# Performance work log

Measured on AMD Instinct MI355X. Metric: run time of the kernel, lower is better.

## Reference

```python
import jax, jax.numpy as jnp
import numpy as np

DIM = 2048
N_HEADS = 16
Q_LORA = 1536
KV_LORA = 512
NOPE = 128
ROPE = 64
QK_D = NOPE + ROPE  # 192
V_D = 128
EPS = 1e-6
B, S = 2, 2048


def rmsnorm(x, w, eps=EPS):
    return x * jax.lax.rsqrt(jnp.mean(x * x, axis=-1, keepdims=True) + eps) * w


def rotate_pe(x, cos, sin):
    # x: [B, S, H, ROPE]; cos/sin: [S, ROPE] -> broadcast [1, S, 1, ROPE]
    c = cos[None, :, None, :]
    s = sin[None, :, None, :]
    x1, x2 = jnp.split(x, 2, axis=-1)
    rot = jnp.concatenate([-x2, x1], axis=-1)
    return x * c + rot * s


def setup_inputs() -> dict:
    key = jax.random.key(0)
    ks = jax.random.split(key, 8)
    std = 0.02
    x = jax.random.normal(ks[0], (B, S, DIM), dtype=jnp.float32)
    # proper rotary tables
    inv_freq = 1.0 / (10000.0 ** (np.arange(0, ROPE, 2, dtype=np.float32) / ROPE))
    t = np.arange(S, dtype=np.float32)
    freqs = np.outer(t, inv_freq)  # [S, ROPE/2]
    emb = np.concatenate([freqs, freqs], axis=-1)  # [S, ROPE]
    cos = jnp.asarray(np.cos(emb))
    sin = jnp.asarray(np.sin(emb))
    wq_a = jax.random.normal(ks[1], (Q_LORA, DIM), dtype=jnp.float32) * std
    q_norm_w = jnp.ones((Q_LORA,), dtype=jnp.float32)
    wq_b = jax.random.normal(ks[2], (N_HEADS * QK_D, Q_LORA), dtype=jnp.float32) * std
    wkv_a = jax.random.normal(ks[3], (KV_LORA + ROPE, DIM), dtype=jnp.float32) * std
    kv_norm_w = jnp.ones((KV_LORA,), dtype=jnp.float32)
    wkv_b = jax.random.normal(ks[4], (N_HEADS * (NOPE + V_D), KV_LORA), dtype=jnp.float32) * std
    wo = jax.random.normal(ks[5], (DIM, N_HEADS * V_D), dtype=jnp.float32) * std
    return {"x": x, "cos": cos, "sin": sin, "wq_a": wq_a, "q_norm_w": q_norm_w,
            "wq_b": wq_b, "wkv_a": wkv_a, "kv_norm_w": kv_norm_w, "wkv_b": wkv_b, "wo": wo}


def mla_forward(x, cos, sin, wq_a, q_norm_w, wq_b, wkv_a, kv_norm_w, wkv_b, wo):
    bsz, seqlen, _ = x.shape
    scale = QK_D ** (-0.5)
    # Q path: low-rank down-proj -> RMSNorm -> up-proj
    q = rmsnorm(x @ wq_a.T, q_norm_w) @ wq_b.T
    q = q.reshape(bsz, seqlen, N_HEADS, QK_D)
    q_nope, q_pe = q[..., :NOPE], q[..., NOPE:]
    q_pe = rotate_pe(q_pe, cos, sin)
    q = jnp.concatenate([q_nope, q_pe], axis=-1)
    # KV path: shared low-rank latent + single rope slice
    kv = x @ wkv_a.T  # [B, S, KV_LORA + ROPE]
    kv_c, k_pe = kv[..., :KV_LORA], kv[..., KV_LORA:]
    k_pe = rotate_pe(k_pe[:, :, None, :], cos, sin)  # [B, S, 1, ROPE]
    kvb = rmsnorm(kv_c, kv_norm_w) @ wkv_b.T
    kvb = kvb.reshape(bsz, seqlen, N_HEADS, NOPE + V_D)
    k_nope, v = kvb[..., :NOPE], kvb[..., NOPE:]
    k = jnp.concatenate([k_nope, jnp.broadcast_to(k_pe, (bsz, seqlen, N_HEADS, ROPE))], axis=-1)
    # causal attention
    scores = jnp.einsum('bqhd,bkhd->bhqk', q, k) * scale
    mask = jnp.tril(jnp.ones((seqlen, seqlen), dtype=bool))
    scores = jnp.where(mask[None, None], scores, jnp.finfo(scores.dtype).min)
    p = jax.nn.softmax(scores, axis=-1)
    out = jnp.einsum('bhqk,bkhd->bqhd', p, v)
    out = out.reshape(bsz, seqlen, N_HEADS * V_D)
    return out @ wo.T


def reference(x, cos, sin, wq_a, q_norm_w, wq_b, wkv_a, kv_norm_w, wkv_b, wo):
    return mla_forward(x, cos, sin, wq_a, q_norm_w, wq_b, wkv_a, kv_norm_w, wkv_b, wo)
```

## Files before the change

### kernel.cpp

```cpp
#include <hip/hip_runtime.h>

typedef unsigned short u16;
typedef __attribute__((ext_vector_type(8))) short short8;
typedef __attribute__((ext_vector_type(4))) float floatx4;

__device__ __forceinline__ float bf2f(u16 u) {
  union { unsigned int i; float f; } v; v.i = ((unsigned int)u) << 16; return v.f;
}
__device__ __forceinline__ u16 f2bf(float f) {
  union { float f; unsigned int i; } v; v.f = f;
  unsigned int u = v.i;
  u += 0x7fffu + ((u >> 16) & 1u);
  return (u16)(u >> 16);
}

__device__ __forceinline__ void gld_lds16(const void* g, void* l) {
  __builtin_amdgcn_global_load_lds(
      (const __attribute__((address_space(1))) unsigned int*)g,
      (__attribute__((address_space(3))) unsigned int*)l, 16, 0, 0);
}

#define SBAR()   __builtin_amdgcn_s_barrier()
#define SCHED0() __builtin_amdgcn_sched_barrier(0)

__global__ __launch_bounds__(256) void repack_all_k(
    const float* __restrict__ x, const float* __restrict__ wqa,
    const float* __restrict__ wkva, const float* __restrict__ wqb,
    const float* __restrict__ wkvb, const float* __restrict__ wo,
    u16* __restrict__ xb, u16* __restrict__ wcat, u16* __restrict__ wqbb,
    u16* __restrict__ wkbb, u16* __restrict__ wob) {
  long i = ((long)blockIdx.x * 256 + threadIdx.x) * 4;
  int region = blockIdx.y;
  const float* s = nullptr; u16* d = nullptr; long n = 0;
  switch (region) {
    case 0: s = x;    d = xb;   n = 4096L * 2048; break;
    case 1: s = nullptr; d = wcat; n = 2176L * 2048; break;
    case 2: s = wqb;  d = wqbb; n = 3072L * 1536; break;
    case 3: s = wkvb; d = wkbb; n = 4096L * 512;  break;
    case 4: s = wo;   d = wob;  n = 2048L * 2048; break;
  }
  if (i >= n) return;
  float4 v;
  if (region == 1) {
    long r = i >> 11, c = i & 2047;
    if (r < 1536)      v = *(const float4*)(wqa + r * 2048 + c);
    else if (r < 2112) v = *(const float4*)(wkva + (r - 1536) * 2048 + c);
    else               v = (float4){0.f, 0.f, 0.f, 0.f};
  } else {
    v = *(const float4*)(s + i);
  }
  d[i + 0] = f2bf(v.x); d[i + 1] = f2bf(v.y);
  d[i + 2] = f2bf(v.z); d[i + 3] = f2bf(v.w);
}

template <int OUT_F32>
__device__ __forceinline__ void gemm_tile(
    const u16* __restrict__ A, int lda, const u16* __restrict__ W, int ldw,
    void* __restrict__ Cv, int ldc, int K, int bm, int bn,
    u16* Asm, u16* Bsm) {
  int tid = threadIdx.x;
  int lane = tid & 63, w = tid >> 6;
  int wm = (w >> 1) * 64, wn = (w & 1) * 64;

  floatx4 acc[4][4];
#pragma unroll
  for (int i = 0; i < 4; i++)
#pragma unroll
    for (int j = 0; j < 4; j++) acc[i][j] = (floatx4){0.f, 0.f, 0.f, 0.f};

  int sr = lane >> 2;
  int sc = (lane & 3) * 8;
  int fr = lane & 15;
  int fq = (lane >> 4) * 8;

  for (int k0 = 0; k0 < K; k0 += 32) {
#pragma unroll
    for (int c = 0; c < 2; c++) {
      int row = 32 * w + 16 * c + sr;
      gld_lds16(A + (size_t)(bm + row) * lda + k0 + sc, &Asm[(32 * w + 16 * c) * 32]);
      gld_lds16(W + (size_t)(bn + row) * ldw + k0 + sc, &Bsm[(32 * w + 16 * c) * 32]);
    }
    __syncthreads();
    short8 af[4], bfr[4];
#pragma unroll
    for (int i = 0; i < 4; i++)
      af[i] = *(const short8*)&Asm[(wm + i * 16 + fr) * 32 + fq];
#pragma unroll
    for (int j = 0; j < 4; j++)
      bfr[j] = *(const short8*)&Bsm[(wn + j * 16 + fr) * 32 + fq];
#pragma unroll
    for (int i = 0; i < 4; i++)
#pragma unroll
      for (int j = 0; j < 4; j++)
        acc[i][j] = __builtin_amdgcn_mfma_f32_16x16x32_bf16(af[i], bfr[j], acc[i][j], 0, 0, 0);
    __syncthreads();
  }

  int cr = (lane >> 4) * 4, cc = lane & 15;
#pragma unroll
  for (int i = 0; i < 4; i++)
#pragma unroll
    for (int j = 0; j < 4; j++) {
      int col = bn + wn + j * 16 + cc;
#pragma unroll
      for (int r = 0; r < 4; r++) {
        size_t row = (size_t)(bm + wm + i * 16 + cr + r);
        if (OUT_F32) ((float*)Cv)[row * ldc + col] = acc[i][j][r];
        else         ((u16*)Cv)[row * ldc + col] = f2bf(acc[i][j][r]);
      }
    }
}

template <int OUT_F32>
__global__ __launch_bounds__(256) void gemm_bt_mfma(
    const u16* __restrict__ A, int lda,
    const u16* __restrict__ W, int ldw,
    void* __restrict__ Cv, int ldc, int K) {
  __shared__ u16 Asm[128 * 32];
  __shared__ u16 Bsm[128 * 32];
  gemm_tile<OUT_F32>(A, lda, W, ldw, Cv, ldc, K, blockIdx.y * 128, blockIdx.x * 128, Asm, Bsm);
}

__global__ __launch_bounds__(256) void gemm_dual_mfma(
    const u16* __restrict__ A1, int lda1, const u16* __restrict__ W1, int ldw1,
    u16* __restrict__ C1, int ldc1, int K1, int nt1,
    const u16* __restrict__ A2, int lda2, const u16* __restrict__ W2, int ldw2,
    u16* __restrict__ C2, int ldc2, int K2) {
  __shared__ u16 Asm[128 * 32];
  __shared__ u16 Bsm[128 * 32];
  int bx = blockIdx.x;
  if (bx < nt1)
    gemm_tile<0>(A1, lda1, W1, ldw1, C1, ldc1, K1, blockIdx.y * 128, bx * 128, Asm, Bsm);
  else
    gemm_tile<0>(A2, lda2, W2, ldw2, C2, ldc2, K2, blockIdx.y * 128, (bx - nt1) * 128, Asm, Bsm);
}

#define GPHASE(LAc, LBc, QQ, STAGE_STMT, WAIT_STMT)                              \
  {                                                                              \
    short8 a00 = *(const short8*)&(LAc)[agbase + (2*(QQ)) * 1024 + g0];          \
    short8 a01 = *(const short8*)&(LAc)[agbase + (2*(QQ)) * 1024 + g1];          \
    short8 a10 = *(const short8*)&(LAc)[agbase + (2*(QQ)+1) * 1024 + g0];        \
    short8 a11 = *(const short8*)&(LAc)[agbase + (2*(QQ)+1) * 1024 + g1];        \
    if ((QQ) == 0) {                                                             \
      _Pragma("unroll")                                                          \
      for (int fj = 0; fj < 4; ++fj) {                                           \
        bfrg[fj][0] = *(const short8*)&(LBc)[bgbase + fj * 1024 + g0];           \
        bfrg[fj][1] = *(const short8*)&(LBc)[bgbase + fj * 1024 + g1];           \
      }                                                                          \
    }                                                                            \
    STAGE_STMT;                                                                  \
    WAIT_STMT;                                                                   \
    SCHED0();                                                                    \
    SBAR();                                                                      \
    asm volatile("s_waitcnt lgkmcnt(0)" ::: "memory");                           \
    SCHED0();                                                                    \
    __builtin_amdgcn_s_setprio(1);                                               \
    _Pragma("unroll")                                                            \
    for (int fj = 0; fj < 4; ++fj) {                                             \
      acc[2*(QQ)][fj]   = __builtin_amdgcn_mfma_f32_16x16x32_bf16(a00, bfrg[fj][0], acc[2*(QQ)][fj],   0, 0, 0); \
      acc[2*(QQ)][fj]   = __builtin_amdgcn_mfma_f32_16x16x32_bf16(a01, bfrg[fj][1], acc[2*(QQ)][fj],   0, 0, 0); \
      acc[2*(QQ)+1][fj] = __builtin_amdgcn_mfma_f32_16x16x32_bf16(a10, bfrg[fj][0], acc[2*(QQ)+1][fj], 0, 0, 0); \
      acc[2*(QQ)+1][fj] = __builtin_amdgcn_mfma_f32_16x16x32_bf16(a11, bfrg[fj][1], acc[2*(QQ)+1][fj], 0, 0, 0); \
    }                                                                            \
    __builtin_amdgcn_s_setprio(0);                                               \
    SCHED0();                                                                    \
    SBAR();                                                                      \
  }

template <int OUT_F32>
__device__ __forceinline__ void gemm256_tile(
    const u16* __restrict__ A, int lda, const u16* __restrict__ W, int ldw,
    void* __restrict__ Cv, int ldc, int K, int bm, int bn,
    u16* __restrict__ LA, u16* __restrict__ LB) {
  int tid = threadIdx.x;
  int lane = tid & 63, w = tid >> 6;
  int wr = w >> 2, wc = w & 3;
  int fr = lane & 15, fq = lane >> 4;

  int srow = lane >> 3;
  int sgl  = (lane & 7) ^ srow;

  int agbase = (wr * 128 + fr) * 64;
  int bgbase = (wc * 64 + fr) * 64;
  int g0 = ((0 * 4 + fq) ^ (fr & 7)) * 8;
  int g1 = ((1 * 4 + fq) ^ (fr & 7)) * 8;

  floatx4 acc[8][4];
#pragma unroll
  for (int i = 0; i < 8; i++)
#pragma unroll
    for (int j = 0; j < 4; j++) acc[i][j] = (floatx4){0.f, 0.f, 0.f, 0.f};

  auto stA = [&](int buf, int kt, int half) {
#pragma unroll
    for (int j = 0; j < 2; ++j) {
      int rbase = half * 128 + (w * 2 + j) * 8;
      gld_lds16(A + (size_t)(bm + rbase + srow) * lda + kt * 64 + sgl * 8,
                (void*)&LA[buf * 16384 + rbase * 64]);
    }
  };
  auto stB = [&](int buf, int kt, int half) {
#pragma unroll
    for (int j = 0; j < 2; ++j) {
      int rbase = half * 128 + (w * 2 + j) * 8;
      gld_lds16(W + (size_t)(bn + rbase + srow) * ldw + kt * 64 + sgl * 8,
                (void*)&LB[buf * 16384 + rbase * 64]);
    }
  };

  const u16* LA0 = LA;           const u16* LB0 = LB;
  const u16* LA1 = LA + 16384;   const u16* LB1 = LB + 16384;

  stB(0, 0, 0); stB(0, 0, 1);
  stA(0, 0, 0); stA(0, 0, 1);
  stB(1, 1, 0); stB(1, 1, 1);
  asm volatile("s_waitcnt vmcnt(4)" ::: "memory");
  SCHED0();
  SBAR();

  int NI = K >> 7;
  for (int i = 0; i < NI; ++i) {
    bool notlast = (i + 1 < NI);
    int t0 = 2 * i;
    {
      short8 bfrg[4][2];
      GPHASE(LA0, LB0, 0, stA(1, t0 + 1, 0), );
      GPHASE(LA0, LB0, 1, stA(1, t0 + 1, 1), );
      GPHASE(LA0, LB0, 2, if (notlast) stB(0, t0 + 2, 0), );
      GPHASE(LA0, LB0, 3, if (notlast) stB(0, t0 + 2, 1),
             if (notlast) { asm volatile("s_waitcnt vmcnt(4)" ::: "memory"); }
             else         { asm volatile("s_waitcnt vmcnt(0)" ::: "memory"); });
    }
    {
      short8 bfrg[4][2];
      GPHASE(LA1, LB1, 0, if (notlast) stA(0, t0 + 2, 0), );
      GPHASE(LA1, LB1, 1, if (notlast) stA(0, t0 + 2, 1), );
      GPHASE(LA1, LB1, 2, if (notlast) stB(1, t0 + 3, 0), );
      GPHASE(LA1, LB1, 3, if (notlast) stB(1, t0 + 3, 1),
             if (notlast) { asm volatile("s_waitcnt vmcnt(4)" ::: "memory"); });
    }
  }

  int cr = (lane >> 4) * 4, cc = lane & 15;
#pragma unroll
  for (int fi = 0; fi < 8; ++fi)
#pragma unroll
    for (int fj = 0; fj < 4; ++fj) {
      int col = bn + wc * 64 + fj * 16 + cc;
#pragma unroll
      for (int r = 0; r < 4; ++r) {
        size_t row = (size_t)(bm + wr * 128 + fi * 16 + cr + r);
        if (OUT_F32) ((float*)Cv)[row * ldc + col] = acc[fi][fj][r];
        else         ((u16*)Cv)[row * ldc + col] = f2bf(acc[fi][fj][r]);
      }
    }
}

template <int OUT_F32>
__global__ __launch_bounds__(512, 2) void gemm256_k(
    const u16* __restrict__ A, int lda,
    const u16* __restrict__ W, int ldw,
    void* __restrict__ Cv, int ldc, int K) {
  __shared__ __align__(16) u16 LAs[2][256 * 64];
  __shared__ __align__(16) u16 LBs[2][256 * 64];
  gemm256_tile<OUT_F32>(A, lda, W, ldw, Cv, ldc, K,
                        blockIdx.y * 256, blockIdx.x * 256, &LAs[0][0], &LBs[0][0]);
}

__global__ __launch_bounds__(256) void normrope_k(
    u16* __restrict__ qkv, const float* __restrict__ qnw,
    const float* __restrict__ kvnw, const float* __restrict__ cosb,
    const float* __restrict__ sinb, int S) {
  int row = blockIdx.x, tid = threadIdx.x;
  u16* p = qkv + (size_t)row * 2176;
  float s1 = 0.f, s2 = 0.f;
#pragma unroll
  for (int it = 0; it < 6; it++) { float v = bf2f(p[tid + 256 * it]); s1 += v * v; }
#pragma unroll
  for (int it = 0; it < 2; it++) { float v = bf2f(p[1536 + tid + 256 * it]); s2 += v * v; }
  for (int off = 32; off > 0; off >>= 1) {
    s1 += __shfl_down(s1, off);
    s2 += __shfl_down(s2, off);
  }
  __shared__ float red1[4], red2[4];
  if ((tid & 63) == 0) { red1[tid >> 6] = s1; red2[tid >> 6] = s2; }
  __syncthreads();
  float inv1 = rsqrtf((red1[0] + red1[1] + red1[2] + red1[3]) / 1536.f + 1e-6f);
  float inv2 = rsqrtf((red2[0] + red2[1] + red2[2] + red2[3]) / 512.f + 1e-6f);
#pragma unroll
  for (int it = 0; it < 6; it++) {
    int i = tid + 256 * it;
    p[i] = f2bf(bf2f(p[i]) * inv1 * qnw[i]);
  }
#pragma unroll
  for (int it = 0; it < 2; it++) {
    int i = tid + 256 * it;
    p[1536 + i] = f2bf(bf2f(p[1536 + i]) * inv2 * kvnw[i]);
  }
  if (tid < 32) {
    int pos = row % S;
    float c1 = cosb[pos * 64 + tid];
    float c2 = cosb[pos * 64 + tid + 32];
    float sn1 = sinb[pos * 64 + tid];
    float sn2 = sinb[pos * 64 + tid + 32];
    float x1 = bf2f(p[2048 + tid]), x2 = bf2f(p[2048 + tid + 32]);
    p[2048 + tid]      = f2bf(x1 * c1 - x2 * sn1);
    p[2048 + tid + 32] = f2bf(x2 * c2 + x1 * sn2);
  }
}

__global__ __launch_bounds__(256) void rope_k(
    u16* __restrict__ base, int row_stride, int head_stride, int head_off,
    const float* __restrict__ cosb, const float* __restrict__ sinb, int S) {
  int t = blockIdx.x;
  int h = blockIdx.y * 8 + (threadIdx.x >> 5);
  int i = threadIdx.x & 31;
  int pos = t % S;
  u16* p = base + (size_t)t * row_stride + h * head_stride + head_off;
  float c1 = cosb[pos * 64 + i];
  float c2 = cosb[pos * 64 + i + 32];
  float s1 = sinb[pos * 64 + i];
  float s2 = sinb[pos * 64 + i + 32];
  float x1 = bf2f(p[i]), x2 = bf2f(p[i + 32]);
  p[i]      = f2bf(x1 * c1 - x2 * s1);
  p[i + 32] = f2bf(x2 * c2 + x1 * s2);
}

__global__ __launch_bounds__(256) void vtrans_k(
    const u16* __restrict__ kvb, u16* __restrict__ vt, int S) {
  int tb = blockIdx.x, h = blockIdx.y, b = blockIdx.z;
  __shared__ __align__(16) u16 Ts[64][136];
  int tid = threadIdx.x;
#pragma unroll
  for (int it = 0; it < 4; it++) {
    int e = tid + 256 * it;
    int tok = e >> 4, c = e & 15;
    short8 v = *(const short8*)(kvb + (size_t)(b * S + tb * 64 + tok) * 4096 + h * 256 + 128 + c * 8);
    *(short8*)&Ts[tok][c * 8] = v;
  }
  __syncthreads();
  int vd = tid >> 1, half = (tid & 1) * 32;
  u16 tmp[32];
#pragma unroll
  for (int j = 0; j < 32; j++) tmp[j] = Ts[half + j][vd];
  u16* dst = vt + ((size_t)((b * 16 + h) * 128) + vd) * S + tb * 64 + half;
#pragma unroll
  for (int c = 0; c < 4; c++)
    *(short8*)(dst + c * 8) = *(short8*)&tmp[c * 8];
}

#define AT_BK 64
__global__ __launch_bounds__(256) void attn_mfma(
    const u16* __restrict__ qf, const u16* __restrict__ kvb,
    const u16* __restrict__ kpe, int kpe_stride, const u16* __restrict__ vt,
    u16* __restrict__ at, int S) {
  int id = blockIdx.x;
  int pair = id >> 5, hb = id & 31;
  int h = hb & 15, b = hb >> 4;
  int NT = S / AT_BK;
  int tid = threadIdx.x, lane = tid & 63, w = tid >> 6;
  int fr = lane & 15, fq = lane >> 4;
  int fs = fr & 7;

  __shared__ __align__(16) u16 Ksn[AT_BK * 128];
  __shared__ __align__(16) u16 Ksp[AT_BK * 64];
  __shared__ __align__(16) u16 Vts[128 * AT_BK];
  __shared__ __align__(16) u16 Ps[64 * AT_BK];

  const float scale = 0.10411804518038971f;

  for (int p = 0; p < 2; p++) {
    int qt = p ? (NT - 1 - pair) : pair;
    int q0 = qt * 64;

    short8 qfrag[6];
    {
      const u16* qrow = qf + (size_t)(b * S + q0 + w * 16 + fr) * 3072 + h * 192 + fq * 8;
#pragma unroll
      for (int ks = 0; ks < 6; ks++) qfrag[ks] = *(const short8*)(qrow + ks * 32);
    }

    floatx4 acc_o[8];
#pragma unroll
    for (int j = 0; j < 8; j++) acc_o[j] = (floatx4){0.f, 0.f, 0.f, 0.f};
    float m_r[4], l_r[4];
#pragma unroll
    for (int r = 0; r < 4; r++) { m_r[r] = -3e38f; l_r[r] = 0.f; }

    for (int kt = 0; kt <= qt; kt++) {
      int k0 = kt * AT_BK;
      size_t tokbase = (size_t)(b * S + k0);
#pragma unroll
      for (int c = 0; c < 4; c++) {
        int row = w * 16 + c * 4 + (lane >> 4);
        int cg = (lane & 15) ^ (row & 7);
        gld_lds16(kvb + (tokbase + row) * 4096 + h * 256 + cg * 8,
                  &Ksn[(w * 16 + c * 4) * 128]);
      }
#pragma unroll
      for (int c = 0; c < 2; c++) {
        int row = w * 16 + c * 8 + (lane >> 3);
        int cg = (lane & 7) ^ (row & 7);
        gld_lds16(kpe + (tokbase + row) * kpe_stride + cg * 8,
                  &Ksp[(w * 16 + c * 8) * 64]);
      }
#pragma unroll
      for (int c = 0; c < 4; c++) {
        int vd = w * 32 + c * 8 + (lane >> 3);
        int cg = (lane & 7) ^ (vd & 7);
        gld_lds16(vt + ((size_t)((b * 16 + h) * 128) + vd) * S + k0 + cg * 8,
                  &Vts[(w * 32 + c * 8) * 64]);
      }
      __syncthreads();

      floatx4 accs[4];
#pragma unroll
      for (int nt = 0; nt < 4; nt++) accs[nt] = (floatx4){0.f, 0.f, 0.f, 0.f};
      __builtin_amdgcn_s_setprio(1);
#pragma unroll
      for (int nt = 0; nt < 4; nt++) {
#pragma unroll
        for (int ks = 0; ks < 4; ks++) {
          short8 bf = *(const short8*)&Ksn[(nt * 16 + fr) * 128 + ((ks * 4 + fq) ^ fs) * 8];
          accs[nt] = __builtin_amdgcn_mfma_f32_16x16x32_bf16(qfrag[ks], bf, accs[nt], 0, 0, 0);
        }
#pragma unroll
        for (int ks = 0; ks < 2; ks++) {
          short8 bf = *(const short8*)&Ksp[(nt * 16 + fr) * 64 + ((ks * 4 + fq) ^ fs) * 8];
          accs[nt] = __builtin_amdgcn_mfma_f32_16x16x32_bf16(qfrag[4 + ks], bf, accs[nt], 0, 0, 0);
        }
      }
      __builtin_amdgcn_s_setprio(0);

      bool diag = (kt == qt);
#pragma unroll
      for (int nt = 0; nt < 4; nt++)
#pragma unroll
        for (int r = 0; r < 4; r++) {
          float s = accs[nt][r] * scale;
          if (diag) {
            int col = nt * 16 + fr;
            int row = fq * 4 + r;
            if (k0 + col > q0 + w * 16 + row) s = -3e38f;
          }
          accs[nt][r] = s;
        }

      float mx4[4];
      int grow = 0;
#pragma unroll
      for (int r = 0; r < 4; r++) {
        float mx = fmaxf(fmaxf(accs[0][r], accs[1][r]), fmaxf(accs[2][r], accs[3][r]));
        mx = fmaxf(mx, __shfl_xor(mx, 1));
        mx = fmaxf(mx, __shfl_xor(mx, 2));
        mx = fmaxf(mx, __shfl_xor(mx, 4));
        mx = fmaxf(mx, __shfl_xor(mx, 8));
        mx4[r] = mx;
        grow |= (mx > m_r[r] + 8.f) ? 1 : 0;
      }
      bool resc = __any(grow);
      float alpha[4];
      if (resc) {
#pragma unroll
        for (int r = 0; r < 4; r++) {
          float mnew = fmaxf(m_r[r], mx4[r]);
          alpha[r] = exp2f(m_r[r] - mnew);
          m_r[r] = mnew;
          l_r[r] *= alpha[r];
        }
      }
#pragma unroll
      for (int nt = 0; nt < 4; nt++)
#pragma unroll
        for (int r = 0; r < 4; r++) {
          float pv = exp2f(accs[nt][r] - m_r[r]);
          l_r[r] += pv;
          int row_p = w * 16 + fq * 4 + r;
          int col = nt * 16 + fr;
          Ps[row_p * 64 + (((col >> 3) ^ (row_p & 7)) * 8) + (col & 7)] = f2bf(pv);
        }
      __syncthreads();

      if (resc) {
#pragma unroll
        for (int j = 0; j < 8; j++)
#pragma unroll
          for (int r = 0; r < 4; r++) acc_o[j][r] *= alpha[r];
      }
      short8 pf0 = *(const short8*)&Ps[(w * 16 + fr) * 64 + (fq ^ fs) * 8];
      short8 pf1 = *(const short8*)&Ps[(w * 16 + fr) * 64 + ((4 + fq) ^ fs) * 8];
      __builtin_amdgcn_s_setprio(1);
#pragma unroll
      for (int j = 0; j < 8; j++) {
        short8 v0 = *(const short8*)&Vts[(j * 16 + fr) * 64 + (fq ^ fs) * 8];
        short8 v1 = *(const short8*)&Vts[(j * 16 + fr) * 64 + ((4 + fq) ^ fs) * 8];
        acc_o[j] = __builtin_amdgcn_mfma_f32_16x16x32_bf16(pf0, v0, acc_o[j], 0, 0, 0);
        acc_o[j] = __builtin_amdgcn_mfma_f32_16x16x32_bf16(pf1, v1, acc_o[j], 0, 0, 0);
      }
      __builtin_amdgcn_s_setprio(0);
      __syncthreads();
    }

    float inv_l[4];
#pragma unroll
    for (int r = 0; r < 4; r++) {
      float sm = l_r[r];
      sm += __shfl_xor(sm, 1);
      sm += __shfl_xor(sm, 2);
      sm += __shfl_xor(sm, 4);
      sm += __shfl_xor(sm, 8);
      inv_l[r] = 1.f / sm;
    }
#pragma unroll
    for (int j = 0; j < 8; j++)
#pragma unroll
      for (int r = 0; r < 4; r++) {
        size_t row = (size_t)(b * S + q0 + w * 16 + fq * 4 + r);
        at[row * 2048 + h * 128 + j * 16 + fr] = f2bf(acc_o[j][r] * inv_l[r]);
      }
  }
}

extern "C" void kernel_launch(void* const* d_in, const int* in_sizes, int n_in,
                              void* d_out, int out_size, void* d_ws, size_t ws_size,
                              hipStream_t stream) {
  (void)in_sizes; (void)n_in; (void)out_size; (void)ws_size;
  const float* x     = (const float*)d_in[0];
  const float* cosb  = (const float*)d_in[1];
  const float* sinb  = (const float*)d_in[2];
  const float* wq_a  = (const float*)d_in[3];
  const float* qnw   = (const float*)d_in[4];
  const float* wq_b  = (const float*)d_in[5];
  const float* wkv_a = (const float*)d_in[6];
  const float* kvnw  = (const float*)d_in[7];
  const float* wkv_b = (const float*)d_in[8];
  const float* wo    = (const float*)d_in[9];
  float* out = (float*)d_out;
  const int B = 2, S = 2048, T = B * S;

  char* wsb = (char*)d_ws;
  size_t off = 0;
  u16* xb   = (u16*)(wsb + off); off += (size_t)T * 2048 * 2;
  u16* wcat = (u16*)(wsb + off); off += (size_t)2176 * 2048 * 2;
  u16* wqbb = (u16*)(wsb + off); off += (size_t)3072 * 1536 * 2;
  u16* wkbb = (u16*)(wsb + off); off += (size_t)4096 * 512 * 2;
  u16* wob  = (u16*)(wsb + off); off += (size_t)2048 * 2048 * 2;
  u16* qkv  = (u16*)(wsb + off); off += (size_t)T * 2176 * 2;
  u16* qf   = (u16*)(wsb + off); off += (size_t)T * 3072 * 2;
  u16* kvb  = (u16*)(wsb + off); off += (size_t)T * 4096 * 2;
  u16* at   = (u16*)(wsb + off); off += (size_t)T * 2048 * 2;
  u16* vt   = xb;

  repack_all_k<<<dim3(8192, 5), 256, 0, stream>>>(
      x, wq_a, wkv_a, wq_b, wkv_b, wo, xb, wcat, wqbb, wkbb, wob);

  gemm_bt_mfma<0><<<dim3(2176 / 128, T / 128), 256, 0, stream>>>(xb, 2048, wcat, 2048, qkv, 2176, 2048);
  normrope_k<<<T, 256, 0, stream>>>(qkv, qnw, kvnw, cosb, sinb, S);
  gemm_dual_mfma<<<dim3(3072 / 128 + 4096 / 128, T / 128), 256, 0, stream>>>(
      qkv, 2176, wqbb, 1536, qf, 3072, 1536, 3072 / 128,
      qkv + 1536, 2176, wkbb, 512, kvb, 4096, 512);
  rope_k<<<dim3(T, 2), 256, 0, stream>>>(qf, 3072, 192, 128, cosb, sinb, S);
  vtrans_k<<<dim3(S / 64, 16, B), 256, 0, stream>>>(kvb, vt, S);
  attn_mfma<<<dim3((S / 128) * 32), 256, 0, stream>>>(qf, kvb, qkv + 2048, 2176, vt, at, S);
  gemm256_k<1><<<dim3(2048 / 256, T / 256), 512, 0, stream>>>(at, 2048, wob, 2048, out, 2048, 2048);
}
```

Before: 480.4 us.

## Double-buffer K/V tiles in attention and reuse rope-K buffer for P

The attention kernel now keeps two LDS buffers for the K-nope, K-rope and V^T tiles. It prefetches the next key tile (or the first tile of the second query tile) with direct global-to-LDS loads while the current tile is being computed. The P matrix is written into the already-consumed K-rope buffer, and the block-wide barrier after the softmax is replaced by a per-wave lgkmcnt wait, since each wave reads back only its own P rows. The softmax switches from exp2f with a log2e-folded scale to __expf with the plain scale, which may add a multiply per exponential. Doubling the LDS footprint could lower occupancy.

```diff
diff --git a/kernel.cpp b/kernel.cpp
--- a/kernel.cpp
+++ b/kernel.cpp
@@ -362,12 +362,43 @@
   int fr = lane & 15, fq = lane >> 4;
   int fs = fr & 7;
 
-  __shared__ __align__(16) u16 Ksn[AT_BK * 128];
-  __shared__ __align__(16) u16 Ksp[AT_BK * 64];
-  __shared__ __align__(16) u16 Vts[128 * AT_BK];
-  __shared__ __align__(16) u16 Ps[64 * AT_BK];
-
-  const float scale = 0.10411804518038971f;
+  __shared__ __align__(16) u16 Ksn[2][AT_BK * 128];
+  __shared__ __align__(16) u16 Ksp[2][AT_BK * 64];
+  __shared__ __align__(16) u16 Vts[2][128 * AT_BK];
+
+  const float scale = 0.07216878364870323f;
+  const size_t vbase = (size_t)((b * 16 + h) * 128);
+
+  auto stage = [&](u16* Kn, u16* Kp, u16* Vt, size_t tokbase, int k0v) {
+#pragma unroll
+    for (int c = 0; c < 4; c++) {
+      int row = w * 16 + c * 4 + (lane >> 4);
+      int cg = (lane & 15) ^ (row & 7);
+      gld_lds16(kvb + (tokbase + row) * 4096 + h * 256 + cg * 8,
+                &Kn[(w * 16 + c * 4) * 128]);
+    }
+#pragma unroll
+    for (int c = 0; c < 2; c++) {
+      int row = w * 16 + c * 8 + (lane >> 3);
+      int cg = (lane & 7) ^ (row & 7);
+      gld_lds16(kpe + (tokbase + row) * kpe_stride + cg * 8,
+                &Kp[(w * 16 + c * 8) * 64]);
+    }
+#pragma unroll
+    for (int c = 0; c < 4; c++) {
+      int vd = w * 32 + c * 8 + (lane >> 3);
+      int cg = (lane & 7) ^ (vd & 7);
+      gld_lds16(vt + (vbase + vd) * S + k0v + cg * 8,
+                &Vt[(w * 32 + c * 8) * 64]);
+    }
+  };
+
+  int cur = 0;
+  stage(Ksn[0], Ksp[0], Vts[0], (size_t)(b * S), 0);
+  asm volatile("s_waitcnt vmcnt(0)" ::: "memory");
+  SCHED0();
+  SBAR();
+  SCHED0();
 
   for (int p = 0; p < 2; p++) {
     int qt = p ? (NT - 1 - pair) : pair;
@@ -389,29 +420,13 @@
 
     for (int kt = 0; kt <= qt; kt++) {
       int k0 = kt * AT_BK;
-      size_t tokbase = (size_t)(b * S + k0);
-#pragma unroll
-      for (int c = 0; c < 4; c++) {
-        int row = w * 16 + c * 4 + (lane >> 4);
-        int cg = (lane & 15) ^ (row & 7);
-        gld_lds16(kvb + (tokbase + row) * 4096 + h * 256 + cg * 8,
-                  &Ksn[(w * 16 + c * 4) * 128]);
-      }
-#pragma unroll
-      for (int c = 0; c < 2; c++) {
-        int row = w * 16 + c * 8 + (lane >> 3);
-        int cg = (lane & 7) ^ (row & 7);
-        gld_lds16(kpe + (tokbase + row) * kpe_stride + cg * 8,
-                  &Ksp[(w * 16 + c * 8) * 64]);
-      }
-#pragma unroll
-      for (int c = 0; c < 4; c++) {
-        int vd = w * 32 + c * 8 + (lane >> 3);
-        int cg = (lane & 7) ^ (vd & 7);
-        gld_lds16(vt + ((size_t)((b * 16 + h) * 128) + vd) * S + k0 + cg * 8,
-                  &Vts[(w * 32 + c * 8) * 64]);
-      }
-      __syncthreads();
+      u16* kn_c = Ksn[cur]; u16* kp_c = Ksp[cur]; u16* vt_c = Vts[cur];
+
+      if (kt < qt)
+        stage(Ksn[cur ^ 1], Ksp[cur ^ 1], Vts[cur ^ 1],
+              (size_t)(b * S + k0 + AT_BK), k0 + AT_BK);
+      else if (p == 0)
+        stage(Ksn[cur ^ 1], Ksp[cur ^ 1], Vts[cur ^ 1], (size_t)(b * S), 0);
 
       floatx4 accs[4];
 #pragma unroll
@@ -421,16 +436,20 @@
       for (int nt = 0; nt < 4; nt++) {
 #pragma unroll
         for (int ks = 0; ks < 4; ks++) {
-          short8 bf = *(const short8*)&Ksn[(nt * 16 + fr) * 128 + ((ks * 4 + fq) ^ fs) * 8];
+          short8 bf = *(const short8*)&kn_c[(nt * 16 + fr) * 128 + ((ks * 4 + fq) ^ fs) * 8];
           accs[nt] = __builtin_amdgcn_mfma_f32_16x16x32_bf16(qfrag[ks], bf, accs[nt], 0, 0, 0);
         }
 #pragma unroll
         for (int ks = 0; ks < 2; ks++) {
-          short8 bf = *(const short8*)&Ksp[(nt * 16 + fr) * 64 + ((ks * 4 + fq) ^ fs) * 8];
+          short8 bf = *(const short8*)&kp_c[(nt * 16 + fr) * 64 + ((ks * 4 + fq) ^ fs) * 8];
           accs[nt] = __builtin_amdgcn_mfma_f32_16x16x32_bf16(qfrag[4 + ks], bf, accs[nt], 0, 0, 0);
         }
       }
       __builtin_amdgcn_s_setprio(0);
+      SCHED0();
+      SBAR();
+      SCHED0();
+      u16* Ps = kp_c;
 
       bool diag = (kt == qt);
 #pragma unroll
@@ -464,7 +483,7 @@
 #pragma unroll
         for (int r = 0; r < 4; r++) {
           float mnew = fmaxf(m_r[r], mx4[r]);
-          alpha[r] = exp2f(m_r[r] - mnew);
+          alpha[r] = __expf(m_r[r] - mnew);
           m_r[r] = mnew;
           l_r[r] *= alpha[r];
         }
@@ -473,13 +492,14 @@
       for (int nt = 0; nt < 4; nt++)
 #pragma unroll
         for (int r = 0; r < 4; r++) {
-          float pv = exp2f(accs[nt][r] - m_r[r]);
+          float pv = __expf(accs[nt][r] - m_r[r]);
           l_r[r] += pv;
           int row_p = w * 16 + fq * 4 + r;
           int col = nt * 16 + fr;
           Ps[row_p * 64 + (((col >> 3) ^ (row_p & 7)) * 8) + (col & 7)] = f2bf(pv);
         }
-      __syncthreads();
+      asm volatile("s_waitcnt lgkmcnt(0)" ::: "memory");
+      SCHED0();
 
       if (resc) {
 #pragma unroll
@@ -492,13 +512,19 @@
       __builtin_amdgcn_s_setprio(1);
 #pragma unroll
       for (int j = 0; j < 8; j++) {
-        short8 v0 = *(const short8*)&Vts[(j * 16 + fr) * 64 + (fq ^ fs) * 8];
-        short8 v1 = *(const short8*)&Vts[(j * 16 + fr) * 64 + ((4 + fq) ^ fs) * 8];
+        short8 v0 = *(const short8*)&vt_c[(j * 16 + fr) * 64 + (fq ^ fs) * 8];
+        short8 v1 = *(const short8*)&vt_c[(j * 16 + fr) * 64 + ((4 + fq) ^ fs) * 8];
         acc_o[j] = __builtin_amdgcn_mfma_f32_16x16x32_bf16(pf0, v0, acc_o[j], 0, 0, 0);
         acc_o[j] = __builtin_amdgcn_mfma_f32_16x16x32_bf16(pf1, v1, acc_o[j], 0, 0, 0);
       }
       __builtin_amdgcn_s_setprio(0);
-      __syncthreads();
+
+      SCHED0();
+      asm volatile("s_waitcnt vmcnt(0)" ::: "memory");
+      SCHED0();
+      SBAR();
+      SCHED0();
+      cur ^= 1;
     }
 
     float inv_l[4];
```

After: 528.4 us. 10.0% more time.

## Prefetch next K/V tiles into LDS during attention compute with split barriers

Applied to the files above, without the earlier changes.

Moves the K-nope/K-pe loads for the next key tile to just after the QK^T MFMAs, and the V loads to just after the PV MFMAs, replacing __syncthreads with explicit waitcnt and s_barrier placement. The aim is to overlap global-to-LDS transfers with softmax and MFMA work instead of stalling at the top of each iteration. It also switches the softmax from a pre-folded log2e scale with exp2f to plain scale with __expf, which adds a multiply per element. The hand-counted vmcnt values and prefetch across passes are fragile if the load counts change.

```diff
diff --git a/kernel.cpp b/kernel.cpp
--- a/kernel.cpp
+++ b/kernel.cpp
@@ -367,7 +367,41 @@
   __shared__ __align__(16) u16 Vts[128 * AT_BK];
   __shared__ __align__(16) u16 Ps[64 * AT_BK];
 
-  const float scale = 0.10411804518038971f;
+  const float scale = 0.07216878364870323f;
+  const size_t vbase = (size_t)((b * 16 + h) * 128);
+
+  auto stageK = [&](size_t tokbase) {
+#pragma unroll
+    for (int c = 0; c < 4; c++) {
+      int row = w * 16 + c * 4 + (lane >> 4);
+      int cg = (lane & 15) ^ (row & 7);
+      gld_lds16(kvb + (tokbase + row) * 4096 + h * 256 + cg * 8,
+                &Ksn[(w * 16 + c * 4) * 128]);
+    }
+#pragma unroll
+    for (int c = 0; c < 2; c++) {
+      int row = w * 16 + c * 8 + (lane >> 3);
+      int cg = (lane & 7) ^ (row & 7);
+      gld_lds16(kpe + (tokbase + row) * kpe_stride + cg * 8,
+                &Ksp[(w * 16 + c * 8) * 64]);
+    }
+  };
+  auto stageV = [&](int k0v) {
+#pragma unroll
+    for (int c = 0; c < 4; c++) {
+      int vd = w * 32 + c * 8 + (lane >> 3);
+      int cg = (lane & 7) ^ (vd & 7);
+      gld_lds16(vt + (vbase + vd) * S + k0v + cg * 8,
+                &Vts[(w * 32 + c * 8) * 64]);
+    }
+  };
+
+  stageK((size_t)(b * S));
+  stageV(0);
+  asm volatile("s_waitcnt vmcnt(0)" ::: "memory");
+  SCHED0();
+  SBAR();
+  SCHED0();
 
   for (int p = 0; p < 2; p++) {
     int qt = p ? (NT - 1 - pair) : pair;
@@ -389,29 +423,8 @@
 
     for (int kt = 0; kt <= qt; kt++) {
       int k0 = kt * AT_BK;
-      size_t tokbase = (size_t)(b * S + k0);
-#pragma unroll
-      for (int c = 0; c < 4; c++) {
-        int row = w * 16 + c * 4 + (lane >> 4);
-        int cg = (lane & 15) ^ (row & 7);
-        gld_lds16(kvb + (tokbase + row) * 4096 + h * 256 + cg * 8,
-                  &Ksn[(w * 16 + c * 4) * 128]);
-      }
-#pragma unroll
-      for (int c = 0; c < 2; c++) {
-        int row = w * 16 + c * 8 + (lane >> 3);
-        int cg = (lane & 7) ^ (row & 7);
-        gld_lds16(kpe + (tokbase + row) * kpe_stride + cg * 8,
-                  &Ksp[(w * 16 + c * 8) * 64]);
-      }
-#pragma unroll
-      for (int c = 0; c < 4; c++) {
-        int vd = w * 32 + c * 8 + (lane >> 3);
-        int cg = (lane & 7) ^ (vd & 7);
-        gld_lds16(vt + ((size_t)((b * 16 + h) * 128) + vd) * S + k0 + cg * 8,
-                  &Vts[(w * 32 + c * 8) * 64]);
-      }
-      __syncthreads();
+      bool more = !(p == 1 && kt == qt);
+      int nk0 = (kt < qt) ? (k0 + AT_BK) : 0;
 
       floatx4 accs[4];
 #pragma unroll
@@ -431,6 +444,12 @@
         }
       }
       __builtin_amdgcn_s_setprio(0);
+      SCHED0();
+      SBAR();
+      SCHED0();
+
+      if (more) stageK((size_t)(b * S + nk0));
+      SCHED0();
 
       bool diag = (kt == qt);
 #pragma unroll
@@ -464,7 +483,7 @@
 #pragma unroll
         for (int r = 0; r < 4; r++) {
           float mnew = fmaxf(m_r[r], mx4[r]);
-          alpha[r] = exp2f(m_r[r] - mnew);
+          alpha[r] = __expf(m_r[r] - mnew);
           m_r[r] = mnew;
           l_r[r] *= alpha[r];
         }
@@ -473,13 +492,20 @@
       for (int nt = 0; nt < 4; nt++)
 #pragma unroll
         for (int r = 0; r < 4; r++) {
-          float pv = exp2f(accs[nt][r] - m_r[r]);
+          float pv = __expf(accs[nt][r] - m_r[r]);
           l_r[r] += pv;
           int row_p = w * 16 + fq * 4 + r;
           int col = nt * 16 + fr;
           Ps[row_p * 64 + (((col >> 3) ^ (row_p & 7)) * 8) + (col & 7)] = f2bf(pv);
         }
-      __syncthreads();
+      asm volatile("s_waitcnt lgkmcnt(0)" ::: "memory");
+      SCHED0();
+
+      if (more) { asm volatile("s_waitcnt vmcnt(6)" ::: "memory"); }
+      else      { asm volatile("s_waitcnt vmcnt(0)" ::: "memory"); }
+      SCHED0();
+      SBAR();
+      SCHED0();
 
       if (resc) {
 #pragma unroll
@@ -498,7 +524,18 @@
         acc_o[j] = __builtin_amdgcn_mfma_f32_16x16x32_bf16(pf1, v1, acc_o[j], 0, 0, 0);
       }
       __builtin_amdgcn_s_setprio(0);
-      __syncthreads();
+      SCHED0();
+      SBAR();
+      SCHED0();
+
+      if (more) {
+        stageV(nk0);
+        SCHED0();
+        asm volatile("s_waitcnt vmcnt(4)" ::: "memory");
+        SCHED0();
+        SBAR();
+        SCHED0();
+      }
     }
 
     float inv_l[4];
```

Measured after the change: 473.7 us. About the same (-1.4%).
